# Performance work log

Hardware: AMD Instinct MI355X
Metric: run time of the kernel (lower is better)

Reference implementation:

```python
import jax, jax.numpy as jnp
import numpy as np

N = 16
FS = 48000
NFFT = FS * 8            # irfft length hard-coded in the module
F = NFFT // 2 + 1        # 192001 frequency sample points
DELAYS = [809, 877, 937, 1049, 1151, 1249, 1373, 1499,
          1617, 1753, 1879, 2003, 2131, 2269, 2393, 2521]
GAIN_PER_SAMPLE = 0.9998


def setup_inputs() -> dict:
    key = jax.random.key(0)
    k1, k2, k3 = jax.random.split(key, 3)
    # frequency sample points on the upper half of the unit circle (rfft bins)
    omega = jnp.linspace(0.0, np.pi, F).astype(jnp.float32)
    x_real = jnp.cos(omega)
    x_imag = jnp.sin(omega)
    B = jax.random.normal(k1, (1, N, 1), dtype=jnp.float32) / N
    C = jax.random.normal(k2, (1, 1, N), dtype=jnp.float32) / N
    X = jax.random.normal(k3, (N, N), dtype=jnp.float32)  # raw Linear weight (pre-parametrization)
    return {"x_real": x_real, "x_imag": x_imag, "B": B, "C": C, "X": X}


def _delays_m():
    # torch does (m - mean)/std then forward undoes it: m = m_norm*std + mean
    m = jnp.asarray(DELAYS, dtype=jnp.float32)
    mStd = jnp.std(m, ddof=1)   # torch.std is unbiased
    mAvr = jnp.mean(m)
    m_norm = (m - mAvr) / mStd
    return m_norm * mStd + mAvr


def reference(x_real, x_imag, B, C, X):
    x = (x_real + 1j * x_imag).astype(jnp.complex64)          # [F]
    # Skew -> matrix_exp parametrization: A = expm(triu(X,1) - triu(X,1)^T), orthogonal
    Au = jnp.triu(X, 1)
    A = jax.scipy.linalg.expm(Au - Au.T)                       # [N, N]
    m = _delays_m()                                            # [N] float delays
    gamma = jnp.asarray(GAIN_PER_SAMPLE, jnp.float32) ** m     # diag of Gamma, [N]
    AG = (A * gamma[None, :]).astype(jnp.complex64)            # A @ diag(gamma), [N, N]
    # D = diag_embed(x[:,None] ** m) ; build (D - A Gamma) fused
    Dd = x[:, None] ** m[None, :]                              # [F, N] complex
    M = Dd[:, :, None] * jnp.eye(N, dtype=jnp.complex64) - AG[None, :, :]  # [F, N, N]
    Bc = B.astype(jnp.complex64)                               # [1, N, 1], broadcasts over F
    Hch = jnp.linalg.solve(M, Bc)                              # [F, N, 1]  == inv(M) @ B
    H = Hch[:, :, 0] * C.astype(jnp.complex64).reshape(1, N)   # [F, N]
    Hs = jnp.sum(H, axis=-1)                                   # [F]
    mask = jnp.where(x == 0, 0.0, 1.0).astype(jnp.complex64)   # H_mask zeroing x==0 bins
    h = jnp.fft.irfft(Hs * mask, n=NFFT)                       # [NFFT] real
    h = h / jnp.max(jnp.abs(h))
    return H, h
```

## Files before the change

### kernel.cpp

```cpp
#include <hip/hip_runtime.h>
#include <math.h>

#define NN 16
#define FF 192001
#define NFFTN 384000
#define N1F 1024
#define N2F 375
#define TWO_PI 6.283185307179586476925286766559

__constant__ float c_delays[16] = {809.f, 877.f, 937.f, 1049.f, 1151.f, 1249.f, 1373.f, 1499.f,
                                   1617.f, 1753.f, 1879.f, 2003.f, 2131.f, 2269.f, 2393.f, 2521.f};
__constant__ int c_idelays[16] = {809, 877, 937, 1049, 1151, 1249, 1373, 1499,
                                  1617, 1753, 1879, 2003, 2131, 2269, 2393, 2521};

typedef float v2f __attribute__((ext_vector_type(2)));

__device__ __forceinline__ float fastrcp(float x) {
#if __has_builtin(__builtin_amdgcn_rcpf)
  return __builtin_amdgcn_rcpf(x);
#else
  return 1.0f / x;
#endif
}

__device__ __forceinline__ float2 cmulf(float2 a, float2 b) {
  return make_float2(a.x * b.x - a.y * b.y, a.x * b.y + a.y * b.x);
}

__global__ void expm_kernel(const float* __restrict__ X, float* __restrict__ AGout,
                            unsigned* __restrict__ mx) {
  if (threadIdx.x == 0) *mx = 0u;
  __shared__ double S[16][16], P[16][16], E[16][16];
  const int i = threadIdx.x >> 4, j = threadIdx.x & 15;
  double xu = (j > i) ? (double)X[i * 16 + j] : 0.0;
  double xl = (i > j) ? (double)X[j * 16 + i] : 0.0;
  double s = (xu - xl) * (1.0 / 256.0);
  S[i][j] = s;
  P[i][j] = s;
  E[i][j] = (i == j ? 1.0 : 0.0) + s;
  __syncthreads();
  for (int k = 2; k <= 24; ++k) {
    double acc = 0.0;
#pragma unroll
    for (int l = 0; l < 16; ++l) acc += P[i][l] * S[l][j];
    acc /= (double)k;
    __syncthreads();
    P[i][j] = acc;
    E[i][j] += acc;
    __syncthreads();
  }
  for (int t = 0; t < 8; ++t) {
    double acc = 0.0;
#pragma unroll
    for (int l = 0; l < 16; ++l) acc += E[i][l] * E[l][j];
    __syncthreads();
    E[i][j] = acc;
    __syncthreads();
  }
  double g = exp((double)c_delays[j] * log(0.9998));
  AGout[i * 16 + j] = (float)(E[i][j] * g);
}

template <int S>
__device__ __forceinline__ v2f bc4(v2f v) {
  v2f o;
  o[0] = __int_as_float(__builtin_amdgcn_ds_swizzle(__float_as_int(v[0]), (S << 5) | 0x1C));
  o[1] = __int_as_float(__builtin_amdgcn_ds_swizzle(__float_as_int(v[1]), (S << 5) | 0x1C));
  return o;
}

template <int K, int C>
struct ColLoop4 {
  static __device__ __forceinline__ void run(
      v2f (&M0)[17], v2f (&M1)[17], v2f (&M2)[17], v2f (&M3)[17],
      v2f f0a, v2f f0b, v2f f1a, v2f f1b, v2f f2a, v2f f2b, v2f f3a, v2f f3b) {
    constexpr int SL = K & 3, S = K >> 2;
    v2f pc;
    if constexpr (SL == 0) pc = bc4<S>(M0[C]);
    else if constexpr (SL == 1) pc = bc4<S>(M1[C]);
    else if constexpr (SL == 2) pc = bc4<S>(M2[C]);
    else pc = bc4<S>(M3[C]);
    v2f pcs = {pc[1], pc[0]};
    M0[C] = __builtin_elementwise_fma(f0a, pc, M0[C]);
    M0[C] = __builtin_elementwise_fma(f0b, pcs, M0[C]);
    M1[C] = __builtin_elementwise_fma(f1a, pc, M1[C]);
    M1[C] = __builtin_elementwise_fma(f1b, pcs, M1[C]);
    M2[C] = __builtin_elementwise_fma(f2a, pc, M2[C]);
    M2[C] = __builtin_elementwise_fma(f2b, pcs, M2[C]);
    M3[C] = __builtin_elementwise_fma(f3a, pc, M3[C]);
    M3[C] = __builtin_elementwise_fma(f3b, pcs, M3[C]);
    ColLoop4<K, C + 1>::run(M0, M1, M2, M3, f0a, f0b, f1a, f1b, f2a, f2b, f3a, f3b);
  }
};
template <int K>
struct ColLoop4<K, 17> {
  static __device__ __forceinline__ void run(v2f (&)[17], v2f (&)[17], v2f (&)[17], v2f (&)[17],
                                             v2f, v2f, v2f, v2f, v2f, v2f, v2f, v2f) {}
};

template <int K>
struct GJStep4 {
  static __device__ __forceinline__ void run(v2f (&M0)[17], v2f (&M1)[17], v2f (&M2)[17],
                                             v2f (&M3)[17], int s) {
    constexpr int SL = K & 3, S = K >> 2;
    v2f pk;
    if constexpr (SL == 0) pk = bc4<S>(M0[K]);
    else if constexpr (SL == 1) pk = bc4<S>(M1[K]);
    else if constexpr (SL == 2) pk = bc4<S>(M2[K]);
    else pk = bc4<S>(M3[K]);
    float invd = fastrcp(pk[0] * pk[0] + pk[1] * pk[1]);
    float rcx = pk[0] * invd, rcy = -pk[1] * invd;
    const bool inS = (s == S);
    v2f m0 = M0[K], m1 = M1[K], m2 = M2[K], m3 = M3[K];
    const bool p0 = inS && (SL == 0), p1 = inS && (SL == 1);
    const bool p2 = inS && (SL == 2), p3 = inS && (SL == 3);
    float f0x = p0 ? (1.0f - rcx) : (m0[0] * rcx - m0[1] * rcy);
    float f0y = p0 ? (-rcy)       : (m0[0] * rcy + m0[1] * rcx);
    float f1x = p1 ? (1.0f - rcx) : (m1[0] * rcx - m1[1] * rcy);
    float f1y = p1 ? (-rcy)       : (m1[0] * rcy + m1[1] * rcx);
    float f2x = p2 ? (1.0f - rcx) : (m2[0] * rcx - m2[1] * rcy);
    float f2y = p2 ? (-rcy)       : (m2[0] * rcy + m2[1] * rcx);
    float f3x = p3 ? (1.0f - rcx) : (m3[0] * rcx - m3[1] * rcy);
    float f3y = p3 ? (-rcy)       : (m3[0] * rcy + m3[1] * rcx);
    ColLoop4<K, K + 1>::run(M0, M1, M2, M3,
                            (v2f){-f0x, -f0x}, (v2f){f0y, -f0y},
                            (v2f){-f1x, -f1x}, (v2f){f1y, -f1y},
                            (v2f){-f2x, -f2x}, (v2f){f2y, -f2y},
                            (v2f){-f3x, -f3x}, (v2f){f3y, -f3y});
    GJStep4<K + 1>::run(M0, M1, M2, M3, s);
  }
};
template <>
struct GJStep4<16> {
  static __device__ __forceinline__ void run(v2f (&)[17], v2f (&)[17], v2f (&)[17], v2f (&)[17], int) {}
};

#define INITROW(Mj, jj, cj, sj)                                                   \
  do {                                                                            \
    const int rr_ = a0 + jj;                                                      \
    float4 q0 = AG4[rr_ * 4 + 0], q1 = AG4[rr_ * 4 + 1];                          \
    float4 q2 = AG4[rr_ * 4 + 2], q3 = AG4[rr_ * 4 + 3];                          \
    Mj[0]  = (v2f){(rr_ == 0  ? cj : 0.0f) - q0.x, (rr_ == 0  ? sj : 0.0f)};      \
    Mj[1]  = (v2f){(rr_ == 1  ? cj : 0.0f) - q0.y, (rr_ == 1  ? sj : 0.0f)};      \
    Mj[2]  = (v2f){(rr_ == 2  ? cj : 0.0f) - q0.z, (rr_ == 2  ? sj : 0.0f)};      \
    Mj[3]  = (v2f){(rr_ == 3  ? cj : 0.0f) - q0.w, (rr_ == 3  ? sj : 0.0f)};      \
    Mj[4]  = (v2f){(rr_ == 4  ? cj : 0.0f) - q1.x, (rr_ == 4  ? sj : 0.0f)};      \
    Mj[5]  = (v2f){(rr_ == 5  ? cj : 0.0f) - q1.y, (rr_ == 5  ? sj : 0.0f)};      \
    Mj[6]  = (v2f){(rr_ == 6  ? cj : 0.0f) - q1.z, (rr_ == 6  ? sj : 0.0f)};      \
    Mj[7]  = (v2f){(rr_ == 7  ? cj : 0.0f) - q1.w, (rr_ == 7  ? sj : 0.0f)};      \
    Mj[8]  = (v2f){(rr_ == 8  ? cj : 0.0f) - q2.x, (rr_ == 8  ? sj : 0.0f)};      \
    Mj[9]  = (v2f){(rr_ == 9  ? cj : 0.0f) - q2.y, (rr_ == 9  ? sj : 0.0f)};      \
    Mj[10] = (v2f){(rr_ == 10 ? cj : 0.0f) - q2.z, (rr_ == 10 ? sj : 0.0f)};      \
    Mj[11] = (v2f){(rr_ == 11 ? cj : 0.0f) - q2.w, (rr_ == 11 ? sj : 0.0f)};      \
    Mj[12] = (v2f){(rr_ == 12 ? cj : 0.0f) - q3.x, (rr_ == 12 ? sj : 0.0f)};      \
    Mj[13] = (v2f){(rr_ == 13 ? cj : 0.0f) - q3.y, (rr_ == 13 ? sj : 0.0f)};      \
    Mj[14] = (v2f){(rr_ == 14 ? cj : 0.0f) - q3.z, (rr_ == 14 ? sj : 0.0f)};      \
    Mj[15] = (v2f){(rr_ == 15 ? cj : 0.0f) - q3.w, (rr_ == 15 ? sj : 0.0f)};      \
    Mj[16] = (v2f){Bs[rr_], 0.0f};                                                \
  } while (0)

template <bool CPLX>
__global__ __launch_bounds__(256, 2) void solve_kernel(
    const float* __restrict__ Bv, const float* __restrict__ Cv,
    const float* __restrict__ AGin, float* __restrict__ Hout,
    float2* __restrict__ G) {
  __shared__ float AGs[16][16];
  __shared__ float Bs[16], Cs[16];
  const int tid = threadIdx.x;
  AGs[tid >> 4][tid & 15] = AGin[tid];
  if (tid < 16) { Bs[tid] = Bv[tid]; Cs[tid] = Cv[tid]; }
  const int s = tid & 3;
  const int a0 = s << 2;
  int f = blockIdx.x * 64 + (tid >> 2);
  const bool active = (f < FF);
  if (!active) f = FF - 1;
  __syncthreads();

  int ph0 = (c_idelays[a0 + 0] * f) % NFFTN;
  int ph1 = (c_idelays[a0 + 1] * f) % NFFTN;
  int ph2 = (c_idelays[a0 + 2] * f) % NFFTN;
  int ph3 = (c_idelays[a0 + 3] * f) % NFFTN;
  const float k2r = (float)(TWO_PI / (double)NFFTN);
  float c0, s0, c1, s1, c2, s2, c3, s3;
  sincosf((float)ph0 * k2r, &s0, &c0);
  sincosf((float)ph1 * k2r, &s1, &c1);
  sincosf((float)ph2 * k2r, &s2, &c2);
  sincosf((float)ph3 * k2r, &s3, &c3);

  const float4* AG4 = (const float4*)&AGs[0][0];
  v2f M0[17], M1[17], M2[17], M3[17];
  INITROW(M0, 0, c0, s0);
  INITROW(M1, 1, c1, s1);
  INITROW(M2, 2, c2, s2);
  INITROW(M3, 3, c3, s3);

  GJStep4<0>::run(M0, M1, M2, M3, s);

  const float cc0 = Cs[a0 + 0], cc1 = Cs[a0 + 1], cc2 = Cs[a0 + 2], cc3 = Cs[a0 + 3];
  v2f h0 = {M0[16][0] * cc0, M0[16][1] * cc0};
  v2f h1 = {M1[16][0] * cc1, M1[16][1] * cc1};
  v2f h2 = {M2[16][0] * cc2, M2[16][1] * cc2};
  v2f h3 = {M3[16][0] * cc3, M3[16][1] * cc3};
  if (active) {
    if (CPLX) {
      float4* dst = (float4*)((float2*)Hout + (size_t)f * 16 + a0);
      dst[0] = (float4){h0[0], h0[1], h1[0], h1[1]};
      dst[1] = (float4){h2[0], h2[1], h3[0], h3[1]};
    } else {
      *(float4*)&Hout[(size_t)f * 16 + a0] = (float4){h0[0], h1[0], h2[0], h3[0]};
    }
  }
  float sx = h0[0] + h1[0] + h2[0] + h3[0];
  float sy = h0[1] + h1[1] + h2[1] + h3[1];
  sx += __shfl_xor(sx, 1, 4); sy += __shfl_xor(sy, 1, 4);
  sx += __shfl_xor(sx, 2, 4); sy += __shfl_xor(sy, 2, 4);
  if (active && s == 0) {
    if (f == 0 || f == 192000) sy = 0.0f;
    G[f] = make_float2(sx, sy);
    if (f > 0 && f < 192000) G[NFFTN - f] = make_float2(sx, -sy);
  }
}

__global__ __launch_bounds__(256) void t1_kernel(const float2* __restrict__ G,
                                                 float2* __restrict__ GT) {
  __shared__ float2 tile[32][33];
  const int k1b = blockIdx.x * 32, k2b = blockIdx.y * 32;
  const int tx = threadIdx.x & 31, ty = threadIdx.x >> 5;
#pragma unroll
  for (int i = 0; i < 4; ++i) {
    int k1 = k1b + ty + 8 * i;
    int k2 = k2b + tx;
    if (k2 < N2F) tile[ty + 8 * i][tx] = G[k2 + N2F * k1];
  }
  __syncthreads();
#pragma unroll
  for (int i = 0; i < 4; ++i) {
    int k2 = k2b + ty + 8 * i;
    int k1 = k1b + tx;
    if (k2 < N2F) GT[k2 * 1024 + k1] = tile[tx][ty + 8 * i];
  }
}

__global__ __launch_bounds__(256) void fftA_kernel(const float2* __restrict__ GT,
                                                   float2* __restrict__ AT) {
  __shared__ float2 buf[2][1024];
  __shared__ float2 wtab[512];
  __shared__ float2 wA[32], wB[32];
  const int k2 = blockIdx.x;
  const int tid = threadIdx.x;
#pragma unroll
  for (int rr = 0; rr < 4; ++rr) {
    int k1 = tid + 256 * rr;
    buf[0][k1] = GT[k2 * 1024 + k1];
  }
  {
    float s_, c_;
    sincosf((float)tid * (float)(TWO_PI / 1024.0), &s_, &c_);
    wtab[tid] = make_float2(c_, s_);
    sincosf((float)(tid + 256) * (float)(TWO_PI / 1024.0), &s_, &c_);
    wtab[tid + 256] = make_float2(c_, s_);
  }
  if (tid < 64) {
    double base = TWO_PI * (double)k2 / (double)NFFTN;
    float s_, c_;
    if (tid < 32) {
      sincosf((float)(base * (double)tid), &s_, &c_);
      wA[tid] = make_float2(c_, s_);
    } else {
      int j = tid - 32;
      sincosf((float)(base * 32.0 * (double)j), &s_, &c_);
      wB[j] = make_float2(c_, s_);
    }
  }
  __syncthreads();
  int src = 0;
#pragma unroll
  for (int st = 0; st < 10; ++st) {
    const int sS = 1 << st;
    const int m = 512 >> st;
#pragma unroll
    for (int rr2 = 0; rr2 < 2; ++rr2) {
      int jj = tid + 256 * rr2;
      int p = jj >> st;
      int q = jj & (sS - 1);
      float2 w = wtab[p << st];
      float2 a = buf[src][q + sS * p];
      float2 b = buf[src][q + sS * (p + m)];
      float2 sum = make_float2(a.x + b.x, a.y + b.y);
      float2 d = make_float2(a.x - b.x, a.y - b.y);
      float2 wd = make_float2(d.x * w.x - d.y * w.y, d.x * w.y + d.y * w.x);
      buf[src ^ 1][q + sS * (2 * p)] = sum;
      buf[src ^ 1][q + sS * (2 * p + 1)] = wd;
    }
    __syncthreads();
    src ^= 1;
  }
#pragma unroll
  for (int rr = 0; rr < 4; ++rr) {
    int t1 = tid + 256 * rr;
    float2 vz = buf[src][t1];
    float2 tw = cmulf(wA[t1 & 31], wB[t1 >> 5]);
    AT[k2 * 1024 + t1] = cmulf(vz, tw);
  }
}

__global__ __launch_bounds__(256) void t2_kernel(const float2* __restrict__ AT,
                                                 float2* __restrict__ Bb) {
  __shared__ float2 tile[32][33];
  const int t1b = blockIdx.x * 32, k2b = blockIdx.y * 32;
  const int tx = threadIdx.x & 31, ty = threadIdx.x >> 5;
#pragma unroll
  for (int i = 0; i < 4; ++i) {
    int k2 = k2b + ty + 8 * i;
    int t1 = t1b + tx;
    if (k2 < N2F) tile[ty + 8 * i][tx] = AT[k2 * 1024 + t1];
  }
  __syncthreads();
#pragma unroll
  for (int i = 0; i < 4; ++i) {
    int t1 = t1b + ty + 8 * i;
    int k2 = k2b + tx;
    if (k2 < N2F) Bb[t1 * N2F + k2] = tile[tx][ty + 8 * i];
  }
}

__global__ __launch_bounds__(384) void fftB_kernel(const float2* __restrict__ Bb,
                                                   float* __restrict__ hout,
                                                   unsigned* __restrict__ mx) {
  __shared__ float2 bv[375];
  __shared__ float2 tw[375];
  __shared__ float2 Y[375];
  __shared__ float wmax[6];
  const int t1 = blockIdx.x;
  const int tid = threadIdx.x;
  if (tid < 375) {
    bv[tid] = Bb[t1 * N2F + tid];
    float ang = (float)(TWO_PI * (double)tid / 375.0);
    float s, c;
    sincosf(ang, &s, &c);
    tw[tid] = make_float2(c, s);
  }
  __syncthreads();
  if (tid < 375) {
    const int a = tid / 15, u = tid - 15 * a;
    float ax = 0.f, ay = 0.f;
    int i15 = 0;
#pragma unroll
    for (int b = 0; b < 15; ++b) {
      float2 x = bv[a + 25 * b];
      float2 w = tw[i15 * 25];
      ax += x.x * w.x - x.y * w.y;
      ay += x.x * w.y + x.y * w.x;
      i15 += u;
      if (i15 >= 15) i15 -= 15;
    }
    Y[tid] = make_float2(ax, ay);
  }
  __syncthreads();
  float m = 0.0f;
  if (tid < 375) {
    const int t = tid;
    const int u = t % 15;
    float acc = 0.f;
    int idx = 0;
#pragma unroll
    for (int a = 0; a < 25; ++a) {
      float2 y = Y[a * 15 + u];
      float2 w = tw[idx];
      acc += y.x * w.x - y.y * w.y;
      idx += t;
      if (idx >= 375) idx -= 375;
    }
    float hv = acc * (1.0f / (float)NFFTN);
    hout[t1 + 1024 * t] = hv;
    m = fabsf(hv);
  }
#pragma unroll
  for (int off = 32; off > 0; off >>= 1) m = fmaxf(m, __shfl_xor(m, off, 64));
  if ((tid & 63) == 0) wmax[tid >> 6] = m;
  __syncthreads();
  if (tid == 0) {
    float mm = wmax[0];
#pragma unroll
    for (int w = 1; w < 6; ++w) mm = fmaxf(mm, wmax[w]);
    atomicMax(mx, __float_as_uint(mm));
  }
}

__global__ void norm_kernel(float* __restrict__ h, const unsigned* __restrict__ mx) {
  int i = blockIdx.x * blockDim.x + threadIdx.x;
  float mv = __uint_as_float(*mx);
  if (i < NFFTN) h[i] = h[i] / mv;
}

extern "C" void kernel_launch(void* const* d_in, const int* in_sizes, int n_in,
                              void* d_out, int out_size, void* d_ws, size_t ws_size,
                              hipStream_t stream) {
  (void)in_sizes; (void)n_in; (void)ws_size;
  const float* Bv = (const float*)d_in[2];
  const float* Cv = (const float*)d_in[3];
  const float* X  = (const float*)d_in[4];
  float* out = (float*)d_out;
  char* ws = (char*)d_ws;
  float2* buf0 = (float2*)(ws);
  float2* buf1 = (float2*)(ws + 3072000);
  unsigned* mx = (unsigned*)(ws + 6144000);
  float*  AGw  = (float*)(ws + 6144064);

  float* htail = out + (out_size - NFFTN);

  expm_kernel<<<1, 256, 0, stream>>>(X, AGw, mx);
  if (out_size >= 2 * FF * NN + NFFTN) {
    solve_kernel<true><<<(FF + 63) / 64, 256, 0, stream>>>(Bv, Cv, AGw, out, buf0);
  } else {
    solve_kernel<false><<<(FF + 63) / 64, 256, 0, stream>>>(Bv, Cv, AGw, out, buf0);
  }
  t1_kernel<<<dim3(32, 12), 256, 0, stream>>>(buf0, buf1);
  fftA_kernel<<<N2F, 256, 0, stream>>>(buf1, buf0);
  t2_kernel<<<dim3(32, 12), 256, 0, stream>>>(buf0, buf1);
  fftB_kernel<<<N1F, 384, 0, stream>>>(buf1, htail, mx);
  norm_kernel<<<1500, 256, 0, stream>>>(htail, mx);
}
```

Baseline: 155.7 us.

## Fuse all stages into one persistent kernel with grid-wide barriers

Replaces the seven launches (expm, solve, two transposes, two FFT passes, normalisation) with one persistent kernel of 512 blocks separated by atomic grid barriers. Each block recomputes the 16x16 matrix exponential locally, the solve stage writes directly in transposed layout so the first transpose disappears, and the second FFT pass reads strided columns so the second transpose disappears too. The aim is to remove launch overhead and two global transpose round-trips. In exchange it relies on all 512 blocks being co-resident, adds a memset, makes every block redo the expm, and leaves the later stages with many idle blocks.

Measured after the change: 388.9 us. 150% more time.

```diff
diff --git a/kernel.cpp b/kernel.cpp
--- a/kernel.cpp
+++ b/kernel.cpp
@@ -6,6 +6,7 @@
 #define NFFTN 384000
 #define N1F 1024
 #define N2F 375
+#define NBLK 512
 #define TWO_PI 6.283185307179586476925286766559
 
 __constant__ float c_delays[16] = {809.f, 877.f, 937.f, 1049.f, 1151.f, 1249.f, 1373.f, 1499.f,
@@ -27,38 +28,21 @@
   return make_float2(a.x * b.x - a.y * b.y, a.x * b.y + a.y * b.x);
 }
 
-__global__ void expm_kernel(const float* __restrict__ X, float* __restrict__ AGout,
-                            unsigned* __restrict__ mx) {
-  if (threadIdx.x == 0) *mx = 0u;
-  __shared__ double S[16][16], P[16][16], E[16][16];
-  const int i = threadIdx.x >> 4, j = threadIdx.x & 15;
-  double xu = (j > i) ? (double)X[i * 16 + j] : 0.0;
-  double xl = (i > j) ? (double)X[j * 16 + i] : 0.0;
-  double s = (xu - xl) * (1.0 / 256.0);
-  S[i][j] = s;
-  P[i][j] = s;
-  E[i][j] = (i == j ? 1.0 : 0.0) + s;
+__device__ __forceinline__ void gbar(unsigned* cnt, unsigned* flag) {
   __syncthreads();
-  for (int k = 2; k <= 24; ++k) {
-    double acc = 0.0;
-#pragma unroll
-    for (int l = 0; l < 16; ++l) acc += P[i][l] * S[l][j];
-    acc /= (double)k;
-    __syncthreads();
-    P[i][j] = acc;
-    E[i][j] += acc;
-    __syncthreads();
-  }
-  for (int t = 0; t < 8; ++t) {
-    double acc = 0.0;
-#pragma unroll
-    for (int l = 0; l < 16; ++l) acc += E[i][l] * E[l][j];
-    __syncthreads();
-    E[i][j] = acc;
-    __syncthreads();
-  }
-  double g = exp((double)c_delays[j] * log(0.9998));
-  AGout[i * 16 + j] = (float)(E[i][j] * g);
+  if (threadIdx.x == 0) {
+    __threadfence();
+    unsigned a = __hip_atomic_fetch_add(cnt, 1u, __ATOMIC_ACQ_REL, __HIP_MEMORY_SCOPE_AGENT);
+    if (a == NBLK - 1) {
+      __hip_atomic_store(flag, 1u, __ATOMIC_RELEASE, __HIP_MEMORY_SCOPE_AGENT);
+    } else {
+      while (__hip_atomic_load(flag, __ATOMIC_ACQUIRE, __HIP_MEMORY_SCOPE_AGENT) == 0u) {
+        __builtin_amdgcn_s_sleep(1);
+      }
+    }
+    __threadfence();
+  }
+  __syncthreads();
 }
 
 template <int S>
@@ -160,237 +144,243 @@
   } while (0)
 
 template <bool CPLX>
-__global__ __launch_bounds__(256, 2) void solve_kernel(
+__global__ __launch_bounds__(256, 2) void mega_kernel(
     const float* __restrict__ Bv, const float* __restrict__ Cv,
-    const float* __restrict__ AGin, float* __restrict__ Hout,
-    float2* __restrict__ G) {
-  __shared__ float AGs[16][16];
-  __shared__ float Bs[16], Cs[16];
+    const float* __restrict__ X, float* __restrict__ Hout,
+    float* __restrict__ htail, float2* __restrict__ GT, float2* __restrict__ AT,
+    unsigned* __restrict__ bar) {
+  __shared__ __align__(16) char smem[21504];
   const int tid = threadIdx.x;
-  AGs[tid >> 4][tid & 15] = AGin[tid];
-  if (tid < 16) { Bs[tid] = Bv[tid]; Cs[tid] = Cv[tid]; }
-  const int s = tid & 3;
-  const int a0 = s << 2;
-  int f = blockIdx.x * 64 + (tid >> 2);
-  const bool active = (f < FF);
-  if (!active) f = FF - 1;
-  __syncthreads();
-
-  int ph0 = (c_idelays[a0 + 0] * f) % NFFTN;
-  int ph1 = (c_idelays[a0 + 1] * f) % NFFTN;
-  int ph2 = (c_idelays[a0 + 2] * f) % NFFTN;
-  int ph3 = (c_idelays[a0 + 3] * f) % NFFTN;
-  const float k2r = (float)(TWO_PI / (double)NFFTN);
-  float c0, s0, c1, s1, c2, s2, c3, s3;
-  sincosf((float)ph0 * k2r, &s0, &c0);
-  sincosf((float)ph1 * k2r, &s1, &c1);
-  sincosf((float)ph2 * k2r, &s2, &c2);
-  sincosf((float)ph3 * k2r, &s3, &c3);
-
-  const float4* AG4 = (const float4*)&AGs[0][0];
-  v2f M0[17], M1[17], M2[17], M3[17];
-  INITROW(M0, 0, c0, s0);
-  INITROW(M1, 1, c1, s1);
-  INITROW(M2, 2, c2, s2);
-  INITROW(M3, 3, c3, s3);
-
-  GJStep4<0>::run(M0, M1, M2, M3, s);
-
-  const float cc0 = Cs[a0 + 0], cc1 = Cs[a0 + 1], cc2 = Cs[a0 + 2], cc3 = Cs[a0 + 3];
-  v2f h0 = {M0[16][0] * cc0, M0[16][1] * cc0};
-  v2f h1 = {M1[16][0] * cc1, M1[16][1] * cc1};
-  v2f h2 = {M2[16][0] * cc2, M2[16][1] * cc2};
-  v2f h3 = {M3[16][0] * cc3, M3[16][1] * cc3};
-  if (active) {
-    if (CPLX) {
-      float4* dst = (float4*)((float2*)Hout + (size_t)f * 16 + a0);
-      dst[0] = (float4){h0[0], h0[1], h1[0], h1[1]};
-      dst[1] = (float4){h2[0], h2[1], h3[0], h3[1]};
-    } else {
-      *(float4*)&Hout[(size_t)f * 16 + a0] = (float4){h0[0], h1[0], h2[0], h3[0]};
-    }
-  }
-  float sx = h0[0] + h1[0] + h2[0] + h3[0];
-  float sy = h0[1] + h1[1] + h2[1] + h3[1];
-  sx += __shfl_xor(sx, 1, 4); sy += __shfl_xor(sy, 1, 4);
-  sx += __shfl_xor(sx, 2, 4); sy += __shfl_xor(sy, 2, 4);
-  if (active && s == 0) {
-    if (f == 0 || f == 192000) sy = 0.0f;
-    G[f] = make_float2(sx, sy);
-    if (f > 0 && f < 192000) G[NFFTN - f] = make_float2(sx, -sy);
-  }
-}
-
-__global__ __launch_bounds__(256) void t1_kernel(const float2* __restrict__ G,
-                                                 float2* __restrict__ GT) {
-  __shared__ float2 tile[32][33];
-  const int k1b = blockIdx.x * 32, k2b = blockIdx.y * 32;
-  const int tx = threadIdx.x & 31, ty = threadIdx.x >> 5;
-#pragma unroll
-  for (int i = 0; i < 4; ++i) {
-    int k1 = k1b + ty + 8 * i;
-    int k2 = k2b + tx;
-    if (k2 < N2F) tile[ty + 8 * i][tx] = G[k2 + N2F * k1];
-  }
-  __syncthreads();
-#pragma unroll
-  for (int i = 0; i < 4; ++i) {
-    int k2 = k2b + ty + 8 * i;
-    int k1 = k1b + tx;
-    if (k2 < N2F) GT[k2 * 1024 + k1] = tile[tx][ty + 8 * i];
-  }
-}
-
-__global__ __launch_bounds__(256) void fftA_kernel(const float2* __restrict__ GT,
-                                                   float2* __restrict__ AT) {
-  __shared__ float2 buf[2][1024];
-  __shared__ float2 wtab[512];
-  __shared__ float2 wA[32], wB[32];
-  const int k2 = blockIdx.x;
-  const int tid = threadIdx.x;
-#pragma unroll
-  for (int rr = 0; rr < 4; ++rr) {
-    int k1 = tid + 256 * rr;
-    buf[0][k1] = GT[k2 * 1024 + k1];
-  }
+  unsigned* mx = bar + 6;
+
   {
-    float s_, c_;
-    sincosf((float)tid * (float)(TWO_PI / 1024.0), &s_, &c_);
-    wtab[tid] = make_float2(c_, s_);
-    sincosf((float)(tid + 256) * (float)(TWO_PI / 1024.0), &s_, &c_);
-    wtab[tid + 256] = make_float2(c_, s_);
-  }
-  if (tid < 64) {
-    double base = TWO_PI * (double)k2 / (double)NFFTN;
-    float s_, c_;
-    if (tid < 32) {
-      sincosf((float)(base * (double)tid), &s_, &c_);
-      wA[tid] = make_float2(c_, s_);
-    } else {
-      int j = tid - 32;
-      sincosf((float)(base * 32.0 * (double)j), &s_, &c_);
-      wB[j] = make_float2(c_, s_);
-    }
-  }
-  __syncthreads();
-  int src = 0;
-#pragma unroll
-  for (int st = 0; st < 10; ++st) {
-    const int sS = 1 << st;
-    const int m = 512 >> st;
-#pragma unroll
-    for (int rr2 = 0; rr2 < 2; ++rr2) {
-      int jj = tid + 256 * rr2;
-      int p = jj >> st;
-      int q = jj & (sS - 1);
-      float2 w = wtab[p << st];
-      float2 a = buf[src][q + sS * p];
-      float2 b = buf[src][q + sS * (p + m)];
-      float2 sum = make_float2(a.x + b.x, a.y + b.y);
-      float2 d = make_float2(a.x - b.x, a.y - b.y);
-      float2 wd = make_float2(d.x * w.x - d.y * w.y, d.x * w.y + d.y * w.x);
-      buf[src ^ 1][q + sS * (2 * p)] = sum;
-      buf[src ^ 1][q + sS * (2 * p + 1)] = wd;
-    }
+    double* S = (double*)smem;
+    double* P = S + 256;
+    double* E = P + 256;
+    float* AGs = (float*)(smem + 8192);
+    float* Bs = (float*)(smem + 9216);
+    float* Cs = (float*)(smem + 9280);
+    if (tid < 16) { Bs[tid] = Bv[tid]; Cs[tid] = Cv[tid]; }
+    const int i = tid >> 4, j = tid & 15;
+    double xu = (j > i) ? (double)X[i * 16 + j] : 0.0;
+    double xl = (i > j) ? (double)X[j * 16 + i] : 0.0;
+    double sv = (xu - xl) * (1.0 / 256.0);
+    S[i * 16 + j] = sv;
+    P[i * 16 + j] = sv;
+    E[i * 16 + j] = (i == j ? 1.0 : 0.0) + sv;
     __syncthreads();
-    src ^= 1;
-  }
-#pragma unroll
-  for (int rr = 0; rr < 4; ++rr) {
-    int t1 = tid + 256 * rr;
-    float2 vz = buf[src][t1];
-    float2 tw = cmulf(wA[t1 & 31], wB[t1 >> 5]);
-    AT[k2 * 1024 + t1] = cmulf(vz, tw);
-  }
-}
-
-__global__ __launch_bounds__(256) void t2_kernel(const float2* __restrict__ AT,
-                                                 float2* __restrict__ Bb) {
-  __shared__ float2 tile[32][33];
-  const int t1b = blockIdx.x * 32, k2b = blockIdx.y * 32;
-  const int tx = threadIdx.x & 31, ty = threadIdx.x >> 5;
-#pragma unroll
-  for (int i = 0; i < 4; ++i) {
-    int k2 = k2b + ty + 8 * i;
-    int t1 = t1b + tx;
-    if (k2 < N2F) tile[ty + 8 * i][tx] = AT[k2 * 1024 + t1];
-  }
-  __syncthreads();
-#pragma unroll
-  for (int i = 0; i < 4; ++i) {
-    int t1 = t1b + ty + 8 * i;
-    int k2 = k2b + tx;
-    if (k2 < N2F) Bb[t1 * N2F + k2] = tile[tx][ty + 8 * i];
-  }
-}
-
-__global__ __launch_bounds__(384) void fftB_kernel(const float2* __restrict__ Bb,
-                                                   float* __restrict__ hout,
-                                                   unsigned* __restrict__ mx) {
-  __shared__ float2 bv[375];
-  __shared__ float2 tw[375];
-  __shared__ float2 Y[375];
-  __shared__ float wmax[6];
-  const int t1 = blockIdx.x;
-  const int tid = threadIdx.x;
-  if (tid < 375) {
-    bv[tid] = Bb[t1 * N2F + tid];
-    float ang = (float)(TWO_PI * (double)tid / 375.0);
-    float s, c;
-    sincosf(ang, &s, &c);
-    tw[tid] = make_float2(c, s);
-  }
-  __syncthreads();
-  if (tid < 375) {
-    const int a = tid / 15, u = tid - 15 * a;
-    float ax = 0.f, ay = 0.f;
-    int i15 = 0;
-#pragma unroll
-    for (int b = 0; b < 15; ++b) {
-      float2 x = bv[a + 25 * b];
-      float2 w = tw[i15 * 25];
-      ax += x.x * w.x - x.y * w.y;
-      ay += x.x * w.y + x.y * w.x;
-      i15 += u;
-      if (i15 >= 15) i15 -= 15;
-    }
-    Y[tid] = make_float2(ax, ay);
-  }
-  __syncthreads();
-  float m = 0.0f;
-  if (tid < 375) {
-    const int t = tid;
-    const int u = t % 15;
-    float acc = 0.f;
-    int idx = 0;
-#pragma unroll
-    for (int a = 0; a < 25; ++a) {
-      float2 y = Y[a * 15 + u];
-      float2 w = tw[idx];
-      acc += y.x * w.x - y.y * w.y;
-      idx += t;
-      if (idx >= 375) idx -= 375;
-    }
-    float hv = acc * (1.0f / (float)NFFTN);
-    hout[t1 + 1024 * t] = hv;
-    m = fabsf(hv);
-  }
-#pragma unroll
-  for (int off = 32; off > 0; off >>= 1) m = fmaxf(m, __shfl_xor(m, off, 64));
-  if ((tid & 63) == 0) wmax[tid >> 6] = m;
-  __syncthreads();
-  if (tid == 0) {
-    float mm = wmax[0];
-#pragma unroll
-    for (int w = 1; w < 6; ++w) mm = fmaxf(mm, wmax[w]);
-    atomicMax(mx, __float_as_uint(mm));
-  }
-}
-
-__global__ void norm_kernel(float* __restrict__ h, const unsigned* __restrict__ mx) {
-  int i = blockIdx.x * blockDim.x + threadIdx.x;
-  float mv = __uint_as_float(*mx);
-  if (i < NFFTN) h[i] = h[i] / mv;
+    for (int k = 2; k <= 24; ++k) {
+      double acc = 0.0;
+#pragma unroll
+      for (int l = 0; l < 16; ++l) acc += P[i * 16 + l] * S[l * 16 + j];
+      acc /= (double)k;
+      __syncthreads();
+      P[i * 16 + j] = acc;
+      E[i * 16 + j] += acc;
+      __syncthreads();
+    }
+    for (int t = 0; t < 8; ++t) {
+      double acc = 0.0;
+#pragma unroll
+      for (int l = 0; l < 16; ++l) acc += E[i * 16 + l] * E[l * 16 + j];
+      __syncthreads();
+      E[i * 16 + j] = acc;
+      __syncthreads();
+    }
+    double g = exp((double)c_delays[j] * log(0.9998));
+    AGs[i * 16 + j] = (float)(E[i * 16 + j] * g);
+    __syncthreads();
+  }
+
+  {
+    const float* AGs = (const float*)(smem + 8192);
+    const float* Bs = (const float*)(smem + 9216);
+    const float* Cs = (const float*)(smem + 9280);
+    const float4* AG4 = (const float4*)AGs;
+    const int s = tid & 3;
+    const int a0 = s << 2;
+    const float k2r = (float)(TWO_PI / (double)NFFTN);
+    for (int vb = blockIdx.x; vb < (FF + 63) / 64; vb += NBLK) {
+      int f = vb * 64 + (tid >> 2);
+      const bool active = (f < FF);
+      if (!active) f = FF - 1;
+      int ph0 = (c_idelays[a0 + 0] * f) % NFFTN;
+      int ph1 = (c_idelays[a0 + 1] * f) % NFFTN;
+      int ph2 = (c_idelays[a0 + 2] * f) % NFFTN;
+      int ph3 = (c_idelays[a0 + 3] * f) % NFFTN;
+      float c0, s0, c1, s1, c2, s2, c3, s3;
+      sincosf((float)ph0 * k2r, &s0, &c0);
+      sincosf((float)ph1 * k2r, &s1, &c1);
+      sincosf((float)ph2 * k2r, &s2, &c2);
+      sincosf((float)ph3 * k2r, &s3, &c3);
+      v2f M0[17], M1[17], M2[17], M3[17];
+      INITROW(M0, 0, c0, s0);
+      INITROW(M1, 1, c1, s1);
+      INITROW(M2, 2, c2, s2);
+      INITROW(M3, 3, c3, s3);
+      GJStep4<0>::run(M0, M1, M2, M3, s);
+      const float cc0 = Cs[a0 + 0], cc1 = Cs[a0 + 1], cc2 = Cs[a0 + 2], cc3 = Cs[a0 + 3];
+      v2f h0 = {M0[16][0] * cc0, M0[16][1] * cc0};
+      v2f h1 = {M1[16][0] * cc1, M1[16][1] * cc1};
+      v2f h2 = {M2[16][0] * cc2, M2[16][1] * cc2};
+      v2f h3 = {M3[16][0] * cc3, M3[16][1] * cc3};
+      if (active) {
+        if (CPLX) {
+          float4* dst = (float4*)((float2*)Hout + (size_t)f * 16 + a0);
+          dst[0] = (float4){h0[0], h0[1], h1[0], h1[1]};
+          dst[1] = (float4){h2[0], h2[1], h3[0], h3[1]};
+        } else {
+          *(float4*)&Hout[(size_t)f * 16 + a0] = (float4){h0[0], h1[0], h2[0], h3[0]};
+        }
+      }
+      float sx = h0[0] + h1[0] + h2[0] + h3[0];
+      float sy = h0[1] + h1[1] + h2[1] + h3[1];
+      sx += __shfl_xor(sx, 1, 4); sy += __shfl_xor(sy, 1, 4);
+      sx += __shfl_xor(sx, 2, 4); sy += __shfl_xor(sy, 2, 4);
+      if (active && s == 0) {
+        if (f == 0 || f == 192000) sy = 0.0f;
+        GT[(f % N2F) * 1024 + f / N2F] = make_float2(sx, sy);
+        if (f > 0 && f < 192000) {
+          int m2 = NFFTN - f;
+          GT[(m2 % N2F) * 1024 + m2 / N2F] = make_float2(sx, -sy);
+        }
+      }
+    }
+  }
+  gbar(bar + 0, bar + 1);
+
+  if (blockIdx.x < N2F) {
+    float2* buf0 = (float2*)smem;
+    float2* buf1 = buf0 + 1024;
+    float2* wtab = (float2*)(smem + 16384);
+    float2* wA = (float2*)(smem + 20480);
+    float2* wB = (float2*)(smem + 20736);
+    const int k2 = blockIdx.x;
+#pragma unroll
+    for (int rr = 0; rr < 4; ++rr) {
+      int k1 = tid + 256 * rr;
+      buf0[k1] = GT[k2 * 1024 + k1];
+    }
+    {
+      float s_, c_;
+      sincosf((float)tid * (float)(TWO_PI / 1024.0), &s_, &c_);
+      wtab[tid] = make_float2(c_, s_);
+      sincosf((float)(tid + 256) * (float)(TWO_PI / 1024.0), &s_, &c_);
+      wtab[tid + 256] = make_float2(c_, s_);
+    }
+    if (tid < 64) {
+      double base = TWO_PI * (double)k2 / (double)NFFTN;
+      float s_, c_;
+      if (tid < 32) {
+        sincosf((float)(base * (double)tid), &s_, &c_);
+        wA[tid] = make_float2(c_, s_);
+      } else {
+        int j = tid - 32;
+        sincosf((float)(base * 32.0 * (double)j), &s_, &c_);
+        wB[j] = make_float2(c_, s_);
+      }
+    }
+    __syncthreads();
+    float2* bsrc = buf0;
+    float2* bdst = buf1;
+#pragma unroll
+    for (int st = 0; st < 10; ++st) {
+      const int sS = 1 << st;
+      const int m = 512 >> st;
+#pragma unroll
+      for (int rr2 = 0; rr2 < 2; ++rr2) {
+        int jj = tid + 256 * rr2;
+        int p = jj >> st;
+        int q = jj & (sS - 1);
+        float2 w = wtab[p << st];
+        float2 a = bsrc[q + sS * p];
+        float2 b = bsrc[q + sS * (p + m)];
+        float2 sum = make_float2(a.x + b.x, a.y + b.y);
+        float2 d = make_float2(a.x - b.x, a.y - b.y);
+        float2 wd = make_float2(d.x * w.x - d.y * w.y, d.x * w.y + d.y * w.x);
+        bdst[q + sS * (2 * p)] = sum;
+        bdst[q + sS * (2 * p + 1)] = wd;
+      }
+      __syncthreads();
+      float2* tmp = bsrc; bsrc = bdst; bdst = tmp;
+    }
+#pragma unroll
+    for (int rr = 0; rr < 4; ++rr) {
+      int t1 = tid + 256 * rr;
+      float2 vz = bsrc[t1];
+      float2 tw = cmulf(wA[t1 & 31], wB[t1 >> 5]);
+      AT[k2 * 1024 + t1] = cmulf(vz, tw);
+    }
+  }
+  gbar(bar + 2, bar + 3);
+
+  {
+    float2* tw = (float2*)smem;
+    float2* bv = (float2*)(smem + 3072);
+    float2* Y  = (float2*)(smem + 6144);
+    float*  wmax = (float*)(smem + 9216);
+    for (int j = tid; j < N2F; j += 256) {
+      float ang = (float)(TWO_PI * (double)j / 375.0);
+      float s_, c_;
+      sincosf(ang, &s_, &c_);
+      tw[j] = make_float2(c_, s_);
+    }
+    float m = 0.0f;
+    for (int t1 = blockIdx.x; t1 < N1F; t1 += NBLK) {
+      __syncthreads();
+      for (int j = tid; j < N2F; j += 256) bv[j] = AT[j * 1024 + t1];
+      __syncthreads();
+      for (int j = tid; j < N2F; j += 256) {
+        const int a = j / 15, u = j - 15 * a;
+        float ax = 0.f, ay = 0.f;
+        int i15 = 0;
+#pragma unroll
+        for (int b = 0; b < 15; ++b) {
+          float2 x = bv[a + 25 * b];
+          float2 w = tw[i15 * 25];
+          ax += x.x * w.x - x.y * w.y;
+          ay += x.x * w.y + x.y * w.x;
+          i15 += u;
+          if (i15 >= 15) i15 -= 15;
+        }
+        Y[j] = make_float2(ax, ay);
+      }
+      __syncthreads();
+      for (int t = tid; t < N2F; t += 256) {
+        const int u = t % 15;
+        float acc = 0.f;
+        int idx = 0;
+#pragma unroll
+        for (int a = 0; a < 25; ++a) {
+          float2 y = Y[a * 15 + u];
+          float2 w = tw[idx];
+          acc += y.x * w.x - y.y * w.y;
+          idx += t;
+          if (idx >= 375) idx -= 375;
+        }
+        float hv = acc * (1.0f / (float)NFFTN);
+        htail[t1 + 1024 * t] = hv;
+        m = fmaxf(m, fabsf(hv));
+      }
+    }
+    __syncthreads();
+#pragma unroll
+    for (int off = 32; off > 0; off >>= 1) m = fmaxf(m, __shfl_xor(m, off, 64));
+    if ((tid & 63) == 0) wmax[tid >> 6] = m;
+    __syncthreads();
+    if (tid == 0) {
+      float mm = fmaxf(fmaxf(wmax[0], wmax[1]), fmaxf(wmax[2], wmax[3]));
+      atomicMax(mx, __float_as_uint(mm));
+    }
+  }
+  gbar(bar + 4, bar + 5);
+
+  {
+    float mv = __uint_as_float(
+        __hip_atomic_load(mx, __ATOMIC_ACQUIRE, __HIP_MEMORY_SCOPE_AGENT));
+    for (int i = blockIdx.x * 256 + tid; i < NFFTN; i += NBLK * 256)
+      htail[i] = htail[i] / mv;
+  }
 }
 
 extern "C" void kernel_launch(void* const* d_in, const int* in_sizes, int n_in,
@@ -402,22 +392,15 @@
   const float* X  = (const float*)d_in[4];
   float* out = (float*)d_out;
   char* ws = (char*)d_ws;
-  float2* buf0 = (float2*)(ws);
-  float2* buf1 = (float2*)(ws + 3072000);
-  unsigned* mx = (unsigned*)(ws + 6144000);
-  float*  AGw  = (float*)(ws + 6144064);
-
+  unsigned* bar = (unsigned*)ws;
+  float2* GT = (float2*)(ws + 1024);
+  float2* AT = (float2*)(ws + 1024 + 3072000);
   float* htail = out + (out_size - NFFTN);
 
-  expm_kernel<<<1, 256, 0, stream>>>(X, AGw, mx);
+  hipMemsetAsync(bar, 0, 64, stream);
   if (out_size >= 2 * FF * NN + NFFTN) {
-    solve_kernel<true><<<(FF + 63) / 64, 256, 0, stream>>>(Bv, Cv, AGw, out, buf0);
+    mega_kernel<true><<<NBLK, 256, 0, stream>>>(Bv, Cv, X, out, htail, GT, AT, bar);
   } else {
-    solve_kernel<false><<<(FF + 63) / 64, 256, 0, stream>>>(Bv, Cv, AGw, out, buf0);
-  }
-  t1_kernel<<<dim3(32, 12), 256, 0, stream>>>(buf0, buf1);
-  fftA_kernel<<<N2F, 256, 0, stream>>>(buf1, buf0);
-  t2_kernel<<<dim3(32, 12), 256, 0, stream>>>(buf0, buf1);
-  fftB_kernel<<<N1F, 384, 0, stream>>>(buf1, htail, mx);
-  norm_kernel<<<1500, 256, 0, stream>>>(htail, mx);
-}
+    mega_kernel<false><<<NBLK, 256, 0, stream>>>(Bv, Cv, X, out, htail, GT, AT, bar);
+  }
+}
```
